# Kernel tuning notes

Hardware: AMD Instinct MI355X
Metric: run time of the kernel (lower is better)

Reference implementation:

```python
import jax, jax.numpy as jnp
import numpy as np

NUM_NODES = 94
SEQ_LEN = 784
OUT_CLASSES = 10
ALPHA = 0.5
GAMMA = 0.1
OMEGA = 2.0 * np.pi / 28.0
H = 1.0
INV_SQRT_N = 1.0 / np.sqrt(NUM_NODES)


def _xavier(key, shape):
    fan_in, fan_out = shape[1], shape[0]
    limit = np.sqrt(6.0 / (fan_in + fan_out))
    return jax.random.uniform(key, shape, jnp.float32, -limit, limit)


def setup_inputs() -> dict:
    key = jax.random.key(0)
    k_in, k_ih, k_hh, k_ro = jax.random.split(key, 4)
    batch = 1024
    return {
        "input_sequence": jax.random.normal(k_in, (batch, SEQ_LEN), jnp.float32),
        "w_ih": _xavier(k_ih, (NUM_NODES, 1)),   # Linear(1 -> N) weight
        "b_ih": jnp.zeros((NUM_NODES,), jnp.float32),
        "w_hh": _xavier(k_hh, (NUM_NODES, NUM_NODES)),  # Linear(N -> N) weight
        "b_hh": jnp.zeros((NUM_NODES,), jnp.float32),
        "w_ro": _xavier(k_ro, (OUT_CLASSES, NUM_NODES)),  # readout weight
        "b_ro": jnp.zeros((OUT_CLASSES,), jnp.float32),
    }


def reference(input_sequence, w_ih, b_ih, w_hh, b_hh, w_ro, b_ro):
    batch = input_sequence.shape[0]
    # precompute external drive for all steps: [T, B, N]
    # W_ih(s_t) with input_dim=1 is an outer product: s_t * w_ih[:,0] + b_ih
    s = input_sequence.T  # [T, B]
    w_ih_vec = w_ih[:, 0]  # [N]

    def step(carry, s_t):
        x, y = carry
        I_ext = s_t[:, None] * w_ih_vec[None, :] + b_ih  # [B, N]
        I_rec = y @ w_hh.T + b_hh                        # [B, N]
        A = (I_ext + I_rec) * INV_SQRT_N
        accel = ALPHA * jnp.tanh(A) - 2.0 * GAMMA * y - (OMEGA ** 2) * x
        x_new = x + H * y
        y_new = y + H * accel
        return (x_new, y_new), None

    x0 = jnp.zeros((batch, NUM_NODES), jnp.float32)
    y0 = jnp.zeros((batch, NUM_NODES), jnp.float32)
    (x_final, _), _ = jax.lax.scan(step, (x0, y0), s)
    return x_final @ w_ro.T + b_ro  # [B, 10]
```

## Files before the change

kernel.cpp:

```cpp
#include <hip/hip_runtime.h>
#include <math.h>

#define NUM_NODES 94
#define SEQ_LEN 784
#define OUT_CLASSES 10

#define TWO_GAMMA 0.2f
#define OM2 0.0503551324598949f
#define INV_SQRT_N 0.103142124625879
#define LOG2E 1.4426950408889634
#define WSCALE ((float)(2.0 * INV_SQRT_N * LOG2E))

typedef _Float16 h2 __attribute__((ext_vector_type(2)));
typedef _Float16 h4 __attribute__((ext_vector_type(4)));
typedef float f2 __attribute__((ext_vector_type(2)));
typedef float f4 __attribute__((ext_vector_type(4)));

__device__ __forceinline__ float dpp_xor1(float x) {
    return __int_as_float(__builtin_amdgcn_mov_dpp(__float_as_int(x), 0xB1, 0xF, 0xF, true));
}
__device__ __forceinline__ float dpp_xor2(float x) {
    return __int_as_float(__builtin_amdgcn_mov_dpp(__float_as_int(x), 0x4E, 0xF, 0xF, true));
}
__device__ __forceinline__ float dpp_mir8(float x) {
    return __int_as_float(__builtin_amdgcn_mov_dpp(__float_as_int(x), 0x141, 0xF, 0xF, true));
}

__device__ __forceinline__ float dot2(h2 a, h2 b, float c) {
#if __has_builtin(__builtin_amdgcn_fdot2)
    return __builtin_amdgcn_fdot2(a, b, c, false);
#else
    return c + (float)a[0] * (float)b[0] + (float)a[1] * (float)b[1];
#endif
}

__global__
__attribute__((amdgpu_flat_work_group_size(64, 64), amdgpu_waves_per_eu(1, 4)))
void horn_kernel(
    const float* __restrict__ input,
    const float* __restrict__ w_ih,
    const float* __restrict__ b_ih,
    const float* __restrict__ w_hh,
    const float* __restrict__ b_hh,
    const float* __restrict__ w_ro,
    const float* __restrict__ b_ro,
    float* __restrict__ out)
{
    __shared__ __align__(16) _Float16 ysh[96];
    __shared__ __align__(16) float    sin_l[SEQ_LEN];
    __shared__ __align__(16) float    xsh[96];

    const int lane = threadIdx.x;
    const int g    = lane >> 3;
    const int lw   = lane & 7;
    const int bb   = blockIdx.x;

    const int b0  = lane & 1, b1 = (lane >> 1) & 1, b2v = (lane >> 2) & 1;
    const int c0i = b0 ^ b2v;
    const int c1i = b1 ^ b2v;
    const int c2i = b2v;

    const int row0 = 12 * g, col0 = 12 * lw;

    {
        const f4* in4 = (const f4*)(input + (size_t)bb * SEQ_LEN);
        f4* s4 = (f4*)sin_l;
        #pragma unroll 1
        for (int i = lane; i < SEQ_LEN / 4; i += 64) s4[i] = in4[i];
    }

    h2 w2[12][6];
    #pragma unroll
    for (int j = 0; j < 12; j++) {
        int rr;
        if (j < 8) {
            rr = row0 + 4 * (((j >> 2) & 1) ^ c2i)
                      + 2 * (((j >> 1) & 1) ^ c1i)
                      +     ((j & 1) ^ c0i);
        } else {
            const int jj = j - 8;
            rr = row0 + 8 + 2 * (((jj >> 1) & 1) ^ c1i)
                          +     ((jj & 1) ^ c0i);
        }
        #pragma unroll
        for (int c = 0; c < 12; c++) {
            const int cc = col0 + c;
            float v = (rr < NUM_NODES && cc < NUM_NODES)
                        ? w_hh[rr * NUM_NODES + cc] * WSCALE : 0.0f;
            w2[j][c >> 1][c & 1] = (_Float16)v;
        }
    }

    const int nA = row0 + 4 * c2i + 2 * c1i + c0i;
    const int nB = row0 + 8 + 2 * c1i + c0i;
    const f2 wih2  = { (nA < NUM_NODES) ? w_ih[nA] * WSCALE : 0.0f,
                       (nB < NUM_NODES) ? w_ih[nB] * WSCALE : 0.0f };
    const f2 bias2 = { (nA < NUM_NODES) ? (b_ih[nA] + b_hh[nA]) * WSCALE : 0.0f,
                       (nB < NUM_NODES) ? (b_ih[nB] + b_hh[nB]) * WSCALE : 0.0f };

    f2 xv = {0.0f, 0.0f};
    f2 yv = {0.0f, 0.0f};

    ysh[nA] = (_Float16)0.0f;
    ysh[nB] = (_Float16)0.0f;
    asm volatile("s_waitcnt lgkmcnt(0) vmcnt(0)" ::: "memory");

    const h4* yv4 = (const h4*)&ysh[col0];

    float st = sin_l[0];

    #pragma unroll 2
    for (int t = 0; t < SEQ_LEN; t++) {
        h4 Y0 = yv4[0], Y1 = yv4[1], Y2 = yv4[2];
        const int tn = (t + 1 < SEQ_LEN) ? t + 1 : (SEQ_LEN - 1);
        float stn = sin_l[tn];
        h2 yy0 = __builtin_shufflevector(Y0, Y0, 0, 1);
        h2 yy1 = __builtin_shufflevector(Y0, Y0, 2, 3);
        h2 yy2 = __builtin_shufflevector(Y1, Y1, 0, 1);
        h2 yy3 = __builtin_shufflevector(Y1, Y1, 2, 3);
        h2 yy4 = __builtin_shufflevector(Y2, Y2, 0, 1);
        h2 yy5 = __builtin_shufflevector(Y2, Y2, 2, 3);

        float P[12];
        #pragma unroll
        for (int i = 0; i < 12; i++) {
            float p = dot2(w2[i][0], yy0, 0.0f);
            p = dot2(w2[i][1], yy1, p);
            p = dot2(w2[i][2], yy2, p);
            p = dot2(w2[i][3], yy3, p);
            p = dot2(w2[i][4], yy4, p);
            p = dot2(w2[i][5], yy5, p);
            P[i] = p;
        }

        float Q0 = P[0]  + dpp_xor1(P[1]);
        float Q1 = P[2]  + dpp_xor1(P[3]);
        float Q2 = P[4]  + dpp_xor1(P[5]);
        float Q3 = P[6]  + dpp_xor1(P[7]);
        float Q4 = P[8]  + dpp_xor1(P[9]);
        float Q5 = P[10] + dpp_xor1(P[11]);
        float R0 = Q0 + dpp_xor2(Q1);
        float R1 = Q2 + dpp_xor2(Q3);
        float R2 = Q4 + dpp_xor2(Q5);
        float SA = R0 + dpp_mir8(R1);
        float SB = R2 + dpp_mir8(R2);

        f2 stv = {st, st};
        f2 Sv  = {SA, SB};
        f2 ev;
        {
            f2 earg = stv * wih2 + bias2 + Sv;
            ev[0] = __builtin_amdgcn_exp2f(earg[0]);
            ev[1] = __builtin_amdgcn_exp2f(earg[1]);
        }
        f2 av;
        av[0] = 0.5f - __builtin_amdgcn_rcpf(ev[0] + 1.0f);
        av[1] = 0.5f - __builtin_amdgcn_rcpf(ev[1] + 1.0f);
        {
            const f2 ng = {-TWO_GAMMA, -TWO_GAMMA};
            const f2 no = {-OM2, -OM2};
            av = ng * yv + av;
            av = no * xv + av;
        }
        xv = xv + yv;
        yv = yv + av;

        ysh[nA] = (_Float16)yv[0];
        ysh[nB] = (_Float16)yv[1];

        st = stn;
    }

    xsh[nA] = xv[0];
    xsh[nB] = xv[1];
    asm volatile("s_waitcnt lgkmcnt(0)" ::: "memory");

    if (lane < OUT_CLASSES) {
        float acc = b_ro[lane];
        #pragma unroll 2
        for (int j = 0; j < NUM_NODES; j++) {
            acc += xsh[j] * w_ro[lane * NUM_NODES + j];
        }
        out[(size_t)bb * OUT_CLASSES + lane] = acc;
    }
}

extern "C" void kernel_launch(void* const* d_in, const int* in_sizes, int n_in,
                              void* d_out, int out_size, void* d_ws, size_t ws_size,
                              hipStream_t stream) {
    const float* input = (const float*)d_in[0];
    const float* w_ih  = (const float*)d_in[1];
    const float* b_ih  = (const float*)d_in[2];
    const float* w_hh  = (const float*)d_in[3];
    const float* b_hh  = (const float*)d_in[4];
    const float* w_ro  = (const float*)d_in[5];
    const float* b_ro  = (const float*)d_in[6];
    float* out = (float*)d_out;

    const int batch = in_sizes[0] / SEQ_LEN;
    dim3 grid(batch);
    dim3 block(64);

    hipLaunchKernelGGL(horn_kernel, grid, block, 0, stream,
                       input, w_ih, b_ih, w_hh, b_hh, w_ro, b_ro, out);
}
```

Measured before the change: 307.1 us.

## Batch 16 sequences per block and compute recurrence with MFMA

New measurement: 293.3 us. 4.5% less time.

```diff
diff --git a/kernel.cpp b/kernel.cpp
--- a/kernel.cpp
+++ b/kernel.cpp
@@ -4,6 +4,10 @@
 #define NUM_NODES 94
 #define SEQ_LEN 784
 #define OUT_CLASSES 10
+#define EPB 16
+#define NW 6
+#define YP 104
+#define SP 796
 
 #define TWO_GAMMA 0.2f
 #define OM2 0.0503551324598949f
@@ -11,31 +15,13 @@
 #define LOG2E 1.4426950408889634
 #define WSCALE ((float)(2.0 * INV_SQRT_N * LOG2E))
 
-typedef _Float16 h2 __attribute__((ext_vector_type(2)));
-typedef _Float16 h4 __attribute__((ext_vector_type(4)));
-typedef float f2 __attribute__((ext_vector_type(2)));
-typedef float f4 __attribute__((ext_vector_type(4)));
-
-__device__ __forceinline__ float dpp_xor1(float x) {
-    return __int_as_float(__builtin_amdgcn_mov_dpp(__float_as_int(x), 0xB1, 0xF, 0xF, true));
-}
-__device__ __forceinline__ float dpp_xor2(float x) {
-    return __int_as_float(__builtin_amdgcn_mov_dpp(__float_as_int(x), 0x4E, 0xF, 0xF, true));
-}
-__device__ __forceinline__ float dpp_mir8(float x) {
-    return __int_as_float(__builtin_amdgcn_mov_dpp(__float_as_int(x), 0x141, 0xF, 0xF, true));
-}
-
-__device__ __forceinline__ float dot2(h2 a, h2 b, float c) {
-#if __has_builtin(__builtin_amdgcn_fdot2)
-    return __builtin_amdgcn_fdot2(a, b, c, false);
-#else
-    return c + (float)a[0] * (float)b[0] + (float)a[1] * (float)b[1];
-#endif
-}
+typedef _Float16 half8 __attribute__((ext_vector_type(8)));
+typedef _Float16 half4 __attribute__((ext_vector_type(4)));
+typedef float    floatx4 __attribute__((ext_vector_type(4)));
+typedef float    f2 __attribute__((ext_vector_type(2)));
 
 __global__
-__attribute__((amdgpu_flat_work_group_size(64, 64), amdgpu_waves_per_eu(1, 4)))
+__attribute__((amdgpu_flat_work_group_size(NW*64, NW*64)))
 void horn_kernel(
     const float* __restrict__ input,
     const float* __restrict__ w_ih,
@@ -46,142 +32,116 @@
     const float* __restrict__ b_ro,
     float* __restrict__ out)
 {
-    __shared__ __align__(16) _Float16 ysh[96];
-    __shared__ __align__(16) float    sin_l[SEQ_LEN];
-    __shared__ __align__(16) float    xsh[96];
+    __shared__ __align__(16) float    sinl[EPB * SP];
+    __shared__ __align__(16) _Float16 ybuf[2][EPB * YP];
 
-    const int lane = threadIdx.x;
-    const int g    = lane >> 3;
-    const int lw   = lane & 7;
+    const int tid  = threadIdx.x;
+    const int m    = tid >> 6;
+    const int lane = tid & 63;
+    const int e    = lane & 15;
+    const int h    = lane >> 4;
     const int bb   = blockIdx.x;
 
-    const int b0  = lane & 1, b1 = (lane >> 1) & 1, b2v = (lane >> 2) & 1;
-    const int c0i = b0 ^ b2v;
-    const int c1i = b1 ^ b2v;
-    const int c2i = b2v;
-
-    const int row0 = 12 * g, col0 = 12 * lw;
-
     {
-        const f4* in4 = (const f4*)(input + (size_t)bb * SEQ_LEN);
-        f4* s4 = (f4*)sin_l;
-        #pragma unroll 1
-        for (int i = lane; i < SEQ_LEN / 4; i += 64) s4[i] = in4[i];
+        const floatx4* in4 = (const floatx4*)(input + (size_t)bb * EPB * SEQ_LEN);
+        for (int idx = tid; idx < EPB * (SEQ_LEN / 4); idx += NW * 64) {
+            int ee = idx / (SEQ_LEN / 4);
+            int cc = idx - ee * (SEQ_LEN / 4);
+            *(floatx4*)&sinl[ee * SP + 4 * cc] = in4[idx];
+        }
+    }
+    {
+        float* yz = (float*)&ybuf[0][0];
+        for (int i = tid; i < (2 * EPB * YP) / 2; i += NW * 64) yz[i] = 0.0f;
     }
 
-    h2 w2[12][6];
+    const int arow = 16 * m + e;
+    half8 a0, a1, a2;
     #pragma unroll
-    for (int j = 0; j < 12; j++) {
-        int rr;
-        if (j < 8) {
-            rr = row0 + 4 * (((j >> 2) & 1) ^ c2i)
-                      + 2 * (((j >> 1) & 1) ^ c1i)
-                      +     ((j & 1) ^ c0i);
-        } else {
-            const int jj = j - 8;
-            rr = row0 + 8 + 2 * (((jj >> 1) & 1) ^ c1i)
-                          +     ((jj & 1) ^ c0i);
-        }
-        #pragma unroll
-        for (int c = 0; c < 12; c++) {
-            const int cc = col0 + c;
-            float v = (rr < NUM_NODES && cc < NUM_NODES)
-                        ? w_hh[rr * NUM_NODES + cc] * WSCALE : 0.0f;
-            w2[j][c >> 1][c & 1] = (_Float16)v;
-        }
+    for (int i = 0; i < 8; i++) {
+        const int kb = 8 * h + i;
+        a0[i] = (_Float16)((arow < NUM_NODES && kb      < NUM_NODES) ? w_hh[arow * NUM_NODES + kb     ] * WSCALE : 0.0f);
+        a1[i] = (_Float16)((arow < NUM_NODES && kb + 32 < NUM_NODES) ? w_hh[arow * NUM_NODES + kb + 32] * WSCALE : 0.0f);
+        a2[i] = (_Float16)((arow < NUM_NODES && kb + 64 < NUM_NODES) ? w_hh[arow * NUM_NODES + kb + 64] * WSCALE : 0.0f);
     }
 
-    const int nA = row0 + 4 * c2i + 2 * c1i + c0i;
-    const int nB = row0 + 8 + 2 * c1i + c0i;
-    const f2 wih2  = { (nA < NUM_NODES) ? w_ih[nA] * WSCALE : 0.0f,
-                       (nB < NUM_NODES) ? w_ih[nB] * WSCALE : 0.0f };
-    const f2 bias2 = { (nA < NUM_NODES) ? (b_ih[nA] + b_hh[nA]) * WSCALE : 0.0f,
-                       (nB < NUM_NODES) ? (b_ih[nB] + b_hh[nB]) * WSCALE : 0.0f };
-
-    f2 xv = {0.0f, 0.0f};
-    f2 yv = {0.0f, 0.0f};
-
-    ysh[nA] = (_Float16)0.0f;
-    ysh[nB] = (_Float16)0.0f;
-    asm volatile("s_waitcnt lgkmcnt(0) vmcnt(0)" ::: "memory");
-
-    const h4* yv4 = (const h4*)&ysh[col0];
-
-    float st = sin_l[0];
-
-    #pragma unroll 2
-    for (int t = 0; t < SEQ_LEN; t++) {
-        h4 Y0 = yv4[0], Y1 = yv4[1], Y2 = yv4[2];
-        const int tn = (t + 1 < SEQ_LEN) ? t + 1 : (SEQ_LEN - 1);
-        float stn = sin_l[tn];
-        h2 yy0 = __builtin_shufflevector(Y0, Y0, 0, 1);
-        h2 yy1 = __builtin_shufflevector(Y0, Y0, 2, 3);
-        h2 yy2 = __builtin_shufflevector(Y1, Y1, 0, 1);
-        h2 yy3 = __builtin_shufflevector(Y1, Y1, 2, 3);
-        h2 yy4 = __builtin_shufflevector(Y2, Y2, 0, 1);
-        h2 yy5 = __builtin_shufflevector(Y2, Y2, 2, 3);
-
-        float P[12];
+    const int r0 = 16 * m + 4 * h;
+    f2 wih01, wih23, bias01, bias23;
+    {
+        float w[4], b[4];
         #pragma unroll
-        for (int i = 0; i < 12; i++) {
-            float p = dot2(w2[i][0], yy0, 0.0f);
-            p = dot2(w2[i][1], yy1, p);
-            p = dot2(w2[i][2], yy2, p);
-            p = dot2(w2[i][3], yy3, p);
-            p = dot2(w2[i][4], yy4, p);
-            p = dot2(w2[i][5], yy5, p);
-            P[i] = p;
+        for (int i = 0; i < 4; i++) {
+            const int r = r0 + i;
+            w[i] = (r < NUM_NODES) ? w_ih[r] * WSCALE : 0.0f;
+            b[i] = (r < NUM_NODES) ? (b_ih[r] + b_hh[r]) * WSCALE : 0.0f;
         }
-
-        float Q0 = P[0]  + dpp_xor1(P[1]);
-        float Q1 = P[2]  + dpp_xor1(P[3]);
-        float Q2 = P[4]  + dpp_xor1(P[5]);
-        float Q3 = P[6]  + dpp_xor1(P[7]);
-        float Q4 = P[8]  + dpp_xor1(P[9]);
-        float Q5 = P[10] + dpp_xor1(P[11]);
-        float R0 = Q0 + dpp_xor2(Q1);
-        float R1 = Q2 + dpp_xor2(Q3);
-        float R2 = Q4 + dpp_xor2(Q5);
-        float SA = R0 + dpp_mir8(R1);
-        float SB = R2 + dpp_mir8(R2);
-
-        f2 stv = {st, st};
-        f2 Sv  = {SA, SB};
-        f2 ev;
-        {
-            f2 earg = stv * wih2 + bias2 + Sv;
-            ev[0] = __builtin_amdgcn_exp2f(earg[0]);
-            ev[1] = __builtin_amdgcn_exp2f(earg[1]);
-        }
-        f2 av;
-        av[0] = 0.5f - __builtin_amdgcn_rcpf(ev[0] + 1.0f);
-        av[1] = 0.5f - __builtin_amdgcn_rcpf(ev[1] + 1.0f);
-        {
-            const f2 ng = {-TWO_GAMMA, -TWO_GAMMA};
-            const f2 no = {-OM2, -OM2};
-            av = ng * yv + av;
-            av = no * xv + av;
-        }
-        xv = xv + yv;
-        yv = yv + av;
-
-        ysh[nA] = (_Float16)yv[0];
-        ysh[nB] = (_Float16)yv[1];
-
-        st = stn;
+        wih01[0] = w[0]; wih01[1] = w[1]; wih23[0] = w[2]; wih23[1] = w[3];
+        bias01[0] = b[0]; bias01[1] = b[1]; bias23[0] = b[2]; bias23[1] = b[3];
     }
 
-    xsh[nA] = xv[0];
-    xsh[nB] = xv[1];
-    asm volatile("s_waitcnt lgkmcnt(0)" ::: "memory");
+    f2 x01 = {0.0f, 0.0f}, x23 = {0.0f, 0.0f};
+    f2 y01 = {0.0f, 0.0f}, y23 = {0.0f, 0.0f};
 
-    if (lane < OUT_CLASSES) {
-        float acc = b_ro[lane];
+    const int rdoff = e * YP + 8 * h;
+    const int wroff = e * YP + r0;
+    const int sbase = e * SP;
+
+    const floatx4 zf4 = {0.0f, 0.0f, 0.0f, 0.0f};
+    const f2 ng = {-TWO_GAMMA, -TWO_GAMMA};
+    const f2 no = {-OM2, -OM2};
+
+    __syncthreads();
+
+    #define HSTEP(RD, WR, T) do {                                                  \
+        half8 b0 = *(const half8*)&(RD)[rdoff];                                    \
+        half8 b1 = *(const half8*)&(RD)[rdoff + 32];                               \
+        half8 b2 = *(const half8*)&(RD)[rdoff + 64];                               \
+        float st = sinl[sbase + (T)];                                              \
+        floatx4 d0 = __builtin_amdgcn_mfma_f32_16x16x32_f16(a0, b0, zf4, 0, 0, 0); \
+        floatx4 d1 = __builtin_amdgcn_mfma_f32_16x16x32_f16(a1, b1, zf4, 0, 0, 0); \
+        floatx4 d2 = __builtin_amdgcn_mfma_f32_16x16x32_f16(a2, b2, zf4, 0, 0, 0); \
+        f2 S01 = { d0[0] + d1[0] + d2[0], d0[1] + d1[1] + d2[1] };                 \
+        f2 S23 = { d0[2] + d1[2] + d2[2], d0[3] + d1[3] + d2[3] };                 \
+        f2 st2 = { st, st };                                                       \
+        f2 e01 = st2 * wih01 + (bias01 + S01);                                     \
+        f2 e23 = st2 * wih23 + (bias23 + S23);                                     \
+        f2 t01, t23;                                                               \
+        t01[0] = 0.5f - __builtin_amdgcn_rcpf(__builtin_amdgcn_exp2f(e01[0]) + 1.0f); \
+        t01[1] = 0.5f - __builtin_amdgcn_rcpf(__builtin_amdgcn_exp2f(e01[1]) + 1.0f); \
+        t23[0] = 0.5f - __builtin_amdgcn_rcpf(__builtin_amdgcn_exp2f(e23[0]) + 1.0f); \
+        t23[1] = 0.5f - __builtin_amdgcn_rcpf(__builtin_amdgcn_exp2f(e23[1]) + 1.0f); \
+        t01 = ng * y01 + t01;  t01 = no * x01 + t01;                               \
+        t23 = ng * y23 + t23;  t23 = no * x23 + t23;                               \
+        x01 += y01;  x23 += y23;                                                   \
+        y01 += t01;  y23 += t23;                                                   \
+        half4 yh;                                                                  \
+        yh[0] = (_Float16)y01[0]; yh[1] = (_Float16)y01[1];                        \
+        yh[2] = (_Float16)y23[0]; yh[3] = (_Float16)y23[1];                        \
+        *(half4*)&(WR)[wroff] = yh;                                                \
+        __syncthreads();                                                           \
+    } while (0)
+
+    for (int t = 0; t < SEQ_LEN; t += 2) {
+        HSTEP(ybuf[0], ybuf[1], t);
+        HSTEP(ybuf[1], ybuf[0], t + 1);
+    }
+    #undef HSTEP
+
+    float* xsh = sinl;
+    {
+        floatx4 xv = { x01[0], x01[1], x23[0], x23[1] };
+        *(floatx4*)&xsh[e * YP + r0] = xv;
+    }
+    __syncthreads();
+
+    if (tid < EPB * OUT_CLASSES) {
+        const int ee = tid / OUT_CLASSES;
+        const int c  = tid - ee * OUT_CLASSES;
+        float acc = b_ro[c];
         #pragma unroll 2
-        for (int j = 0; j < NUM_NODES; j++) {
-            acc += xsh[j] * w_ro[lane * NUM_NODES + j];
-        }
-        out[(size_t)bb * OUT_CLASSES + lane] = acc;
+        for (int r = 0; r < NUM_NODES; r++)
+            acc += xsh[ee * YP + r] * w_ro[c * NUM_NODES + r];
+        out[((size_t)bb * EPB + ee) * OUT_CLASSES + c] = acc;
     }
 }
 
@@ -198,8 +158,8 @@
     float* out = (float*)d_out;
 
     const int batch = in_sizes[0] / SEQ_LEN;
-    dim3 grid(batch);
-    dim3 block(64);
+    dim3 grid(batch / EPB);
+    dim3 block(NW * 64);
 
     hipLaunchKernelGGL(horn_kernel, grid, block, 0, stream,
                        input, w_ih, b_ih, w_hh, b_hh, w_ro, b_ro, out);
```
